# Kernel optimization log

Measured on AMD Instinct MI355X. Metric: run time of the kernel, lower is better.

Reference implementation:

```python
import jax, jax.numpy as jnp
import numpy as np
from jax import lax

# quantization bit widths (config)
IB, WB, RB, AB = 8, 4, 4, 8


def quantize(x, bw):
    """Signed fixed-point quantization to bw bits in [-1, 1) with STE."""
    scale = 2.0 ** (bw - 1)
    q = jnp.clip(jnp.round(x * scale), -scale, scale - 1) / scale
    return x + lax.stop_gradient(q - x)


def setup_inputs() -> dict:
    key = jax.random.key(0)
    k1, k2, k3, k4, k5 = jax.random.split(key, 5)
    B, T, I, H, O = 256, 1024, 64, 256, 16
    inputs = jax.random.normal(k1, (B, T, I), dtype=jnp.float32)
    # input kernel init: uniform(-1, 1)
    Wi = jax.random.uniform(k2, (H, I), dtype=jnp.float32, minval=-1.0, maxval=1.0)
    # recurrent kernel: orthogonal (geotorch parametrization); materialize via QR
    A = jax.random.normal(k3, (H, H), dtype=jnp.float32)
    Wr, _ = jnp.linalg.qr(A)
    Wr = Wr.astype(jnp.float32)
    Wo = jax.random.normal(k4, (O, H), dtype=jnp.float32) * 0.1
    b = jax.random.normal(k5, (H,), dtype=jnp.float32) * 0.01
    return {"inputs": inputs, "Wi": Wi, "Wr": Wr, "Wo": Wo, "b": b}


def reference(inputs, Wi, Wr, Wo, b):
    # quantize inputs (ib bits)
    x = quantize(inputs, IB)
    # quantized input projection, precomputed for all timesteps: [B,T,H]
    u = jnp.einsum("bti,hi->bth", x, quantize(Wi, WB))
    Wrq = quantize(Wr, RB)  # quantized orthogonal recurrent weight [H,H]
    B = inputs.shape[0]
    H = Wr.shape[0]
    h0 = jnp.zeros((B, H), dtype=inputs.dtype)

    def step(h, u_t):
        z = u_t + h @ Wrq.T                      # [B,H]
        m = jax.nn.relu(jnp.abs(z) + b)          # modrelu magnitude
        h_new = quantize(jnp.sign(z) * m, AB)    # quantized activation
        return h_new, None

    u_t = jnp.swapaxes(u, 0, 1)  # [T,B,H]
    h_last, _ = lax.scan(step, h0, u_t)
    # output head on last hidden state
    out = h_last @ quantize(Wo, WB).T  # [B,O]
    return out
```

## Files before the change

kernel.cpp:

```cpp
#include <hip/hip_runtime.h>


#define TSEQ 1024
#define IDIM 64
#define HDIM 256
#define ODIM 16
#define CHUNK 16
#define NCHUNK (TSEQ / CHUNK)

__device__ __forceinline__ int sdot4i8(int a, int b, int c) {
#if __has_builtin(__builtin_amdgcn_sdot4)
    return __builtin_amdgcn_sdot4(a, b, c, false);
#else
    int r = c;
    r += ((a << 24) >> 24) * ((b << 24) >> 24);
    r += ((a << 16) >> 24) * ((b << 16) >> 24);
    r += ((a << 8)  >> 24) * ((b << 8)  >> 24);
    r += (a >> 24) * (b >> 24);
    return r;
#endif
}

__device__ __forceinline__ int qpack4(float4 f, float s, float lo, float hi) {
    int a = (int)fminf(fmaxf(rintf(f.x * s), lo), hi);
    int b = (int)fminf(fmaxf(rintf(f.y * s), lo), hi);
    int c = (int)fminf(fmaxf(rintf(f.z * s), lo), hi);
    int d = (int)fminf(fmaxf(rintf(f.w * s), lo), hi);
    return (a & 255) | ((b & 255) << 8) | ((c & 255) << 16) | ((d & 255) << 24);
}

__global__ __launch_bounds__(256, 1)
void qornn_kernel(const float* __restrict__ x, const float* __restrict__ Wi,
                  const float* __restrict__ Wr, const float* __restrict__ Wo,
                  const float* __restrict__ bias, float* __restrict__ out) {
    __shared__ alignas(16) int wstage[8192];
    __shared__ alignas(16) int xbuf[2][256];
    __shared__ alignas(16) int hbuf[2][64];

    const int tid = threadIdx.x;
    const int brow = blockIdx.x;

    {
        const float4* wi4 = (const float4*)Wi;
        #pragma unroll
        for (int it = 0; it < 16; ++it) {
            int flat = it * 256 + tid;
            wstage[flat] = qpack4(wi4[flat], 8.0f, -8.0f, 7.0f);
        }
    }
    __syncthreads();
    int4 wiq[4];
    {
        const int4* p = (const int4*)wstage;
        #pragma unroll
        for (int i = 0; i < 4; ++i) wiq[i] = p[tid * 4 + i];
    }
    __syncthreads();

    int4 wq[16];
    {
        const float4* wr4 = (const float4*)Wr;
        #pragma unroll
        for (int it = 0; it < 32; ++it) {
            int flat = it * 256 + tid;
            wstage[flat] = qpack4(wr4[flat], 8.0f, -8.0f, 7.0f);
        }
        __syncthreads();
        if (tid < 128) {
            const int4* p = (const int4*)wstage;
            #pragma unroll
            for (int i = 0; i < 16; ++i) wq[i] = p[tid * 16 + i];
        }
        __syncthreads();
        #pragma unroll
        for (int it = 0; it < 32; ++it) {
            int flat = it * 256 + tid;
            wstage[flat] = qpack4(wr4[8192 + flat], 8.0f, -8.0f, 7.0f);
        }
        __syncthreads();
        if (tid >= 128) {
            const int4* p = (const int4*)wstage;
            #pragma unroll
            for (int i = 0; i < 16; ++i) wq[i] = p[(tid - 128) * 16 + i];
        }
        __syncthreads();
    }

    {
        const float4* wo4 = (const float4*)Wo;
        #pragma unroll
        for (int it = 0; it < 4; ++it) {
            int flat = it * 256 + tid;
            wstage[flat] = qpack4(wo4[flat], 8.0f, -8.0f, 7.0f);
        }
    }

    const float bv = bias[tid];

    const float4* rowf4 = (const float4*)(x + (size_t)brow * (TSEQ * IDIM));
    {
        float4 xf = rowf4[tid];
        xbuf[0][tid] = qpack4(xf, 128.0f, -128.0f, 127.0f);
        if (tid < 64) hbuf[0][tid] = 0;
    }
    __syncthreads();

    for (int c = 0; c < NCHUNK; ++c) {
        float4 nf;
        if (c < NCHUNK - 1) nf = rowf4[(c + 1) * 256 + tid];
        const int xb = c & 1;
        const int* xbase = xbuf[xb];

        #pragma unroll
        for (int s = 0; s < CHUNK; ++s) {
            const int pb = s & 1;
            int4 hh[16];
            {
                const int4* hP = (const int4*)hbuf[pb];
                #pragma unroll
                for (int i = 0; i < 16; ++i) hh[i] = hP[i];
            }
            int4 xx[4];
            {
                const int4* xP = (const int4*)(xbase + s * 16);
                #pragma unroll
                for (int i = 0; i < 4; ++i) xx[i] = xP[i];
            }
            int a0 = 0, a1 = 0, a2 = 0, a3 = 0;
            #pragma unroll
            for (int i = 0; i < 16; ++i) {
                a0 = sdot4i8(hh[i].x, wq[i].x, a0);
                a1 = sdot4i8(hh[i].y, wq[i].y, a1);
                a2 = sdot4i8(hh[i].z, wq[i].z, a2);
                a3 = sdot4i8(hh[i].w, wq[i].w, a3);
            }
            #pragma unroll
            for (int i = 0; i < 4; ++i) {
                a0 = sdot4i8(xx[i].x, wiq[i].x, a0);
                a1 = sdot4i8(xx[i].y, wiq[i].y, a1);
                a2 = sdot4i8(xx[i].z, wiq[i].z, a2);
                a3 = sdot4i8(xx[i].w, wiq[i].w, a3);
            }
            const int z = (a0 + a1) + (a2 + a3);

            const float zf = (float)z * 0.0009765625f;
            const float t1 = fabsf(zf) + bv;
            const float t2 = fmaxf(t1, 0.0f);
            const float r  = rintf(t2 * 128.0f);
            const float rp = fminf(r, 127.0f);
            const float rn = fminf(r, 128.0f);
            int hnew = (z < 0) ? -(int)rn : (int)rp;
            hnew = (z == 0) ? 0 : hnew;

            ((signed char*)hbuf[pb ^ 1])[tid] = (signed char)hnew;

            if (s == CHUNK - 1 && c < NCHUNK - 1) {
                xbuf[xb ^ 1][tid] = qpack4(nf, 128.0f, -128.0f, 127.0f);
            }
            __syncthreads();
        }
    }

    if (tid < ODIM) {
        const int4* wo = (const int4*)wstage;
        const int4* hl = (const int4*)hbuf[0];
        int a0 = 0, a1 = 0, a2 = 0, a3 = 0;
        #pragma unroll
        for (int i = 0; i < 16; ++i) {
            int4 w4 = wo[tid * 16 + i];
            int4 h4 = hl[i];
            a0 = sdot4i8(h4.x, w4.x, a0);
            a1 = sdot4i8(h4.y, w4.y, a1);
            a2 = sdot4i8(h4.z, w4.z, a2);
            a3 = sdot4i8(h4.w, w4.w, a3);
        }
        out[brow * ODIM + tid] = (float)((a0 + a1) + (a2 + a3)) * 0.0009765625f;
    }
}

extern "C" void kernel_launch(void* const* d_in, const int* in_sizes, int n_in,
                              void* d_out, int out_size, void* d_ws, size_t ws_size,
                              hipStream_t stream) {
    const float* x  = (const float*)d_in[0];
    const float* Wi = (const float*)d_in[1];
    const float* Wr = (const float*)d_in[2];
    const float* Wo = (const float*)d_in[3];
    const float* b  = (const float*)d_in[4];
    float* out = (float*)d_out;

    const int B = in_sizes[0] / (TSEQ * IDIM);
    qornn_kernel<<<B, HDIM, 0, stream>>>(x, Wi, Wr, Wo, b, out);
}
```

Before: 496.6 us.

## Split each output row's dot product across a lane quad with DPP reduction

Each thread now computes 4 hidden outputs over a quarter of the K dimension instead of 1 output over the full K, and the 4 partials are combined with DPP quad-reduction. Each thread reads only 4 int4 of the hidden state from LDS per step instead of 16, cutting LDS read traffic per step. Each quad writes its 4 results as one packed int. The cost is extra DPP shuffle and add instructions, plus every quad lane repeating the activation math for the 4 outputs.

```diff
diff --git a/kernel.cpp b/kernel.cpp
--- a/kernel.cpp
+++ b/kernel.cpp
@@ -29,6 +29,12 @@
     return (a & 255) | ((b & 255) << 8) | ((c & 255) << 16) | ((d & 255) << 24);
 }
 
+__device__ __forceinline__ int quad_reduce_add(int v) {
+    v += __builtin_amdgcn_update_dpp(0, v, 0xB1, 0xF, 0xF, true);
+    v += __builtin_amdgcn_update_dpp(0, v, 0x4E, 0xF, 0xF, true);
+    return v;
+}
+
 __global__ __launch_bounds__(256, 1)
 void qornn_kernel(const float* __restrict__ x, const float* __restrict__ Wi,
                   const float* __restrict__ Wr, const float* __restrict__ Wo,
@@ -39,6 +45,11 @@
 
     const int tid = threadIdx.x;
     const int brow = blockIdx.x;
+    const int w    = tid >> 6;
+    const int l    = tid & 63;
+    const int q    = l & 3;
+    const int m16  = l >> 2;
+    const int obase = w * 64 + m16 * 4;
 
     {
         const float4* wi4 = (const float4*)Wi;
@@ -53,11 +64,11 @@
     {
         const int4* p = (const int4*)wstage;
         #pragma unroll
-        for (int i = 0; i < 4; ++i) wiq[i] = p[tid * 4 + i];
+        for (int i = 0; i < 4; ++i) wiq[i] = p[(obase + i) * 4 + q];
     }
     __syncthreads();
 
-    int4 wq[16];
+    int4 wr[16];
     {
         const float4* wr4 = (const float4*)Wr;
         #pragma unroll
@@ -66,10 +77,13 @@
             wstage[flat] = qpack4(wr4[flat], 8.0f, -8.0f, 7.0f);
         }
         __syncthreads();
-        if (tid < 128) {
+        if (obase < 128) {
             const int4* p = (const int4*)wstage;
             #pragma unroll
-            for (int i = 0; i < 16; ++i) wq[i] = p[tid * 16 + i];
+            for (int i = 0; i < 4; ++i)
+                #pragma unroll
+                for (int r = 0; r < 4; ++r)
+                    wr[i * 4 + r] = p[(obase + i) * 16 + q * 4 + r];
         }
         __syncthreads();
         #pragma unroll
@@ -78,10 +92,13 @@
             wstage[flat] = qpack4(wr4[8192 + flat], 8.0f, -8.0f, 7.0f);
         }
         __syncthreads();
-        if (tid >= 128) {
+        if (obase >= 128) {
             const int4* p = (const int4*)wstage;
             #pragma unroll
-            for (int i = 0; i < 16; ++i) wq[i] = p[(tid - 128) * 16 + i];
+            for (int i = 0; i < 4; ++i)
+                #pragma unroll
+                for (int r = 0; r < 4; ++r)
+                    wr[i * 4 + r] = p[(obase - 128 + i) * 16 + q * 4 + r];
         }
         __syncthreads();
     }
@@ -95,7 +112,8 @@
         }
     }
 
-    const float bv = bias[tid];
+    const float4 bv4 = *(const float4*)(bias + obase);
+    const float bvv[4] = {bv4.x, bv4.y, bv4.z, bv4.w};
 
     const float4* rowf4 = (const float4*)(x + (size_t)brow * (TSEQ * IDIM));
     {
@@ -114,45 +132,49 @@
         #pragma unroll
         for (int s = 0; s < CHUNK; ++s) {
             const int pb = s & 1;
-            int4 hh[16];
+            int4 hh[4];
             {
                 const int4* hP = (const int4*)hbuf[pb];
                 #pragma unroll
-                for (int i = 0; i < 16; ++i) hh[i] = hP[i];
-            }
-            int4 xx[4];
-            {
-                const int4* xP = (const int4*)(xbase + s * 16);
-                #pragma unroll
-                for (int i = 0; i < 4; ++i) xx[i] = xP[i];
-            }
-            int a0 = 0, a1 = 0, a2 = 0, a3 = 0;
-            #pragma unroll
-            for (int i = 0; i < 16; ++i) {
-                a0 = sdot4i8(hh[i].x, wq[i].x, a0);
-                a1 = sdot4i8(hh[i].y, wq[i].y, a1);
-                a2 = sdot4i8(hh[i].z, wq[i].z, a2);
-                a3 = sdot4i8(hh[i].w, wq[i].w, a3);
+                for (int r = 0; r < 4; ++r) hh[r] = hP[q * 4 + r];
+            }
+            const int4 xx = ((const int4*)(xbase + s * 16))[q];
+
+            int acc[4] = {0, 0, 0, 0};
+            #pragma unroll
+            for (int r = 0; r < 4; ++r) {
+                #pragma unroll
+                for (int i = 0; i < 4; ++i) {
+                    const int4 wv = wr[i * 4 + r];
+                    acc[i] = sdot4i8(hh[r].x, wv.x, acc[i]);
+                    acc[i] = sdot4i8(hh[r].y, wv.y, acc[i]);
+                    acc[i] = sdot4i8(hh[r].z, wv.z, acc[i]);
+                    acc[i] = sdot4i8(hh[r].w, wv.w, acc[i]);
+                }
             }
             #pragma unroll
             for (int i = 0; i < 4; ++i) {
-                a0 = sdot4i8(xx[i].x, wiq[i].x, a0);
-                a1 = sdot4i8(xx[i].y, wiq[i].y, a1);
-                a2 = sdot4i8(xx[i].z, wiq[i].z, a2);
-                a3 = sdot4i8(xx[i].w, wiq[i].w, a3);
-            }
-            const int z = (a0 + a1) + (a2 + a3);
-
-            const float zf = (float)z * 0.0009765625f;
-            const float t1 = fabsf(zf) + bv;
-            const float t2 = fmaxf(t1, 0.0f);
-            const float r  = rintf(t2 * 128.0f);
-            const float rp = fminf(r, 127.0f);
-            const float rn = fminf(r, 128.0f);
-            int hnew = (z < 0) ? -(int)rn : (int)rp;
-            hnew = (z == 0) ? 0 : hnew;
-
-            ((signed char*)hbuf[pb ^ 1])[tid] = (signed char)hnew;
+                acc[i] = sdot4i8(xx.x, wiq[i].x, acc[i]);
+                acc[i] = sdot4i8(xx.y, wiq[i].y, acc[i]);
+                acc[i] = sdot4i8(xx.z, wiq[i].z, acc[i]);
+                acc[i] = sdot4i8(xx.w, wiq[i].w, acc[i]);
+            }
+
+            int packed = 0;
+            #pragma unroll
+            for (int i = 0; i < 4; ++i) {
+                const int z = quad_reduce_add(acc[i]);
+                const float zf = (float)z;
+                const float t1 = fmaf(fabsf(zf), 0.0009765625f, bvv[i]);
+                const float t2 = fmaxf(t1, 0.0f);
+                const float r  = rintf(t2 * 128.0f);
+                const float rp = fminf(r, 127.0f);
+                const float rn = fminf(r, 128.0f);
+                int v = (z < 0) ? -(int)rn : (int)rp;
+                v = (z == 0) ? 0 : v;
+                packed |= (v & 255) << (8 * i);
+            }
+            if (q == 0) hbuf[pb ^ 1][w * 16 + m16] = packed;
 
             if (s == CHUNK - 1 && c < NCHUNK - 1) {
                 xbuf[xb ^ 1][tid] = qpack4(nf, 128.0f, -128.0f, 127.0f);
```

Result: slower. 516.9 us (+4.1%).

## Use int8 MFMA for recurrent matvec and preload quantized sequence into LDS

Applied to the files above, without the earlier changes.

Replaces the per-thread sdot4 dot products with 16x16x64 int8 MFMA instructions, where each wave computes a 64-column slice of the hidden update and the relevant lane pulls its column result. The whole quantized input row (1024 timesteps) is staged once in LDS, replacing the chunked double-buffered prefetch. The next step's input projection is issued as MFMAs off the critical path. It trades redundant MFMA rows (only one row of the 16x16 tile is useful) and a much larger LDS footprint for fewer instructions on the serial per-step dependency chain.

```diff
diff --git a/kernel.cpp b/kernel.cpp
--- a/kernel.cpp
+++ b/kernel.cpp
@@ -5,8 +5,8 @@
 #define IDIM 64
 #define HDIM 256
 #define ODIM 16
-#define CHUNK 16
-#define NCHUNK (TSEQ / CHUNK)
+
+typedef int v4i __attribute__((ext_vector_type(4)));
 
 __device__ __forceinline__ int sdot4i8(int a, int b, int c) {
 #if __has_builtin(__builtin_amdgcn_sdot4)
@@ -33,12 +33,17 @@
 void qornn_kernel(const float* __restrict__ x, const float* __restrict__ Wi,
                   const float* __restrict__ Wr, const float* __restrict__ Wo,
                   const float* __restrict__ bias, float* __restrict__ out) {
+    __shared__ alignas(16) int xlds[TSEQ * 16 + 16];
     __shared__ alignas(16) int wstage[8192];
-    __shared__ alignas(16) int xbuf[2][256];
+    __shared__ alignas(16) int wo_lds[1024];
     __shared__ alignas(16) int hbuf[2][64];
 
     const int tid = threadIdx.x;
     const int brow = blockIdx.x;
+    const int w = tid >> 6;
+    const int l = tid & 63;
+    const int g = l >> 4;
+    const int n = l & 15;
 
     {
         const float4* wi4 = (const float4*)Wi;
@@ -49,41 +54,34 @@
         }
     }
     __syncthreads();
-    int4 wiq[4];
-    {
-        const int4* p = (const int4*)wstage;
-        #pragma unroll
-        for (int i = 0; i < 4; ++i) wiq[i] = p[tid * 4 + i];
-    }
+    v4i wiB[4];
+    #pragma unroll
+    for (int t4 = 0; t4 < 4; ++t4)
+        wiB[t4] = *(const v4i*)(wstage + (w * 64 + t4 * 16 + n) * 16 + g * 4);
     __syncthreads();
 
-    int4 wq[16];
+    v4i wrB[16];
     {
         const float4* wr4 = (const float4*)Wr;
         #pragma unroll
-        for (int it = 0; it < 32; ++it) {
-            int flat = it * 256 + tid;
-            wstage[flat] = qpack4(wr4[flat], 8.0f, -8.0f, 7.0f);
+        for (int half = 0; half < 2; ++half) {
+            #pragma unroll
+            for (int it = 0; it < 32; ++it) {
+                int flat = it * 256 + tid;
+                wstage[flat] = qpack4(wr4[half * 8192 + flat], 8.0f, -8.0f, 7.0f);
+            }
+            __syncthreads();
+            if ((w >> 1) == half) {
+                const int rl = (w & 1) * 64;
+                #pragma unroll
+                for (int t4 = 0; t4 < 4; ++t4)
+                    #pragma unroll
+                    for (int j = 0; j < 4; ++j)
+                        wrB[t4 * 4 + j] =
+                            *(const v4i*)(wstage + (rl + t4 * 16 + n) * 64 + j * 16 + g * 4);
+            }
+            __syncthreads();
         }
-        __syncthreads();
-        if (tid < 128) {
-            const int4* p = (const int4*)wstage;
-            #pragma unroll
-            for (int i = 0; i < 16; ++i) wq[i] = p[tid * 16 + i];
-        }
-        __syncthreads();
-        #pragma unroll
-        for (int it = 0; it < 32; ++it) {
-            int flat = it * 256 + tid;
-            wstage[flat] = qpack4(wr4[8192 + flat], 8.0f, -8.0f, 7.0f);
-        }
-        __syncthreads();
-        if (tid >= 128) {
-            const int4* p = (const int4*)wstage;
-            #pragma unroll
-            for (int i = 0; i < 16; ++i) wq[i] = p[(tid - 128) * 16 + i];
-        }
-        __syncthreads();
     }
 
     {
@@ -91,78 +89,74 @@
         #pragma unroll
         for (int it = 0; it < 4; ++it) {
             int flat = it * 256 + tid;
-            wstage[flat] = qpack4(wo4[flat], 8.0f, -8.0f, 7.0f);
+            wo_lds[flat] = qpack4(wo4[flat], 8.0f, -8.0f, 7.0f);
         }
     }
 
-    const float bv = bias[tid];
-
-    const float4* rowf4 = (const float4*)(x + (size_t)brow * (TSEQ * IDIM));
     {
-        float4 xf = rowf4[tid];
-        xbuf[0][tid] = qpack4(xf, 128.0f, -128.0f, 127.0f);
-        if (tid < 64) hbuf[0][tid] = 0;
+        const float4* rowf4 = (const float4*)(x + (size_t)brow * (TSEQ * IDIM));
+        #pragma unroll 8
+        for (int it = 0; it < 64; ++it) {
+            int flat = it * 256 + tid;
+            xlds[flat] = qpack4(rowf4[flat], 128.0f, -128.0f, 127.0f);
+        }
     }
+    if (tid < 64) hbuf[0][tid] = 0;
     __syncthreads();
 
-    for (int c = 0; c < NCHUNK; ++c) {
-        float4 nf;
-        if (c < NCHUNK - 1) nf = rowf4[(c + 1) * 256 + tid];
-        const int xb = c & 1;
-        const int* xbase = xbuf[xb];
+    const float bv128 = bias[tid] * 128.0f;
+    const v4i zero4 = {0, 0, 0, 0};
 
+    v4i accp[4];
+    {
+        const v4i xA = *(const v4i*)(xlds + g * 4);
         #pragma unroll
-        for (int s = 0; s < CHUNK; ++s) {
-            const int pb = s & 1;
-            int4 hh[16];
-            {
-                const int4* hP = (const int4*)hbuf[pb];
-                #pragma unroll
-                for (int i = 0; i < 16; ++i) hh[i] = hP[i];
-            }
-            int4 xx[4];
-            {
-                const int4* xP = (const int4*)(xbase + s * 16);
-                #pragma unroll
-                for (int i = 0; i < 4; ++i) xx[i] = xP[i];
-            }
-            int a0 = 0, a1 = 0, a2 = 0, a3 = 0;
+        for (int t4 = 0; t4 < 4; ++t4)
+            accp[t4] = __builtin_amdgcn_mfma_i32_16x16x64_i8(xA, wiB[t4], zero4, 0, 0, 0);
+    }
+
+    #pragma unroll 2
+    for (int t = 0; t < TSEQ; ++t) {
+        const char* hsrc = (const char*)hbuf[t & 1];
+        v4i hA[4];
+        #pragma unroll
+        for (int j = 0; j < 4; ++j)
+            hA[j] = *(const v4i*)(hsrc + j * 64 + g * 16);
+
+        v4i acc[4];
+        #pragma unroll
+        for (int t4 = 0; t4 < 4; ++t4) {
+            acc[t4] = accp[t4];
             #pragma unroll
-            for (int i = 0; i < 16; ++i) {
-                a0 = sdot4i8(hh[i].x, wq[i].x, a0);
-                a1 = sdot4i8(hh[i].y, wq[i].y, a1);
-                a2 = sdot4i8(hh[i].z, wq[i].z, a2);
-                a3 = sdot4i8(hh[i].w, wq[i].w, a3);
-            }
-            #pragma unroll
-            for (int i = 0; i < 4; ++i) {
-                a0 = sdot4i8(xx[i].x, wiq[i].x, a0);
-                a1 = sdot4i8(xx[i].y, wiq[i].y, a1);
-                a2 = sdot4i8(xx[i].z, wiq[i].z, a2);
-                a3 = sdot4i8(xx[i].w, wiq[i].w, a3);
-            }
-            const int z = (a0 + a1) + (a2 + a3);
+            for (int j = 0; j < 4; ++j)
+                acc[t4] = __builtin_amdgcn_mfma_i32_16x16x64_i8(hA[j], wrB[t4 * 4 + j],
+                                                                acc[t4], 0, 0, 0);
+        }
 
-            const float zf = (float)z * 0.0009765625f;
-            const float t1 = fabsf(zf) + bv;
-            const float t2 = fmaxf(t1, 0.0f);
-            const float r  = rintf(t2 * 128.0f);
-            const float rp = fminf(r, 127.0f);
-            const float rn = fminf(r, 128.0f);
-            int hnew = (z < 0) ? -(int)rn : (int)rp;
-            hnew = (z == 0) ? 0 : hnew;
+        const int zz = (g == 0) ? acc[0].x : (g == 1) ? acc[1].x
+                     : (g == 2) ? acc[2].x : acc[3].x;
 
-            ((signed char*)hbuf[pb ^ 1])[tid] = (signed char)hnew;
+        const float zf = (float)zz;
+        const float t1 = fmaf(fabsf(zf), 0.125f, bv128);
+        const float t2 = fmaxf(t1, 0.0f);
+        const float r  = rintf(t2);
+        const int vpos = (int)fminf(r, 127.0f);
+        const int vneg = -(int)fminf(r, 128.0f);
+        int hv = (zz < 0) ? vneg : vpos;
+        hv = (zz == 0) ? 0 : hv;
 
-            if (s == CHUNK - 1 && c < NCHUNK - 1) {
-                xbuf[xb ^ 1][tid] = qpack4(nf, 128.0f, -128.0f, 127.0f);
-            }
-            __syncthreads();
-        }
+        ((signed char*)hbuf[(t + 1) & 1])[tid] = (signed char)hv;
+
+        const v4i xA = *(const v4i*)(xlds + (t + 1) * 16 + g * 4);
+        #pragma unroll
+        for (int t4 = 0; t4 < 4; ++t4)
+            accp[t4] = __builtin_amdgcn_mfma_i32_16x16x64_i8(xA, wiB[t4], zero4, 0, 0, 0);
+
+        __syncthreads();
     }
 
     if (tid < ODIM) {
-        const int4* wo = (const int4*)wstage;
+        const int4* wo = (const int4*)wo_lds;
         const int4* hl = (const int4*)hbuf[0];
         int a0 = 0, a1 = 0, a2 = 0, a3 = 0;
         #pragma unroll
```

Measured after the change: 428.3 us. 13.7% less time.
